# Kernel optimization log

Measured on AMD Instinct MI355X. Metric: run time of the kernel, lower is better.

The kernel has to match this reference:

```python
import jax, jax.numpy as jnp
import numpy as np

HID, D, NH, NL = 1024, 64, 16, 128  # hidden_dim, head_dim, num_head, num_landmarks


def iterative_inv(mat, n_iter=6):
    # Moore-Penrose pseudo-inverse via Newton-Schulz (Nystromformer), fp32.
    I = jnp.eye(mat.shape[-1], dtype=mat.dtype)
    K = mat
    denom = (jnp.max(jnp.sum(jnp.abs(K), axis=-2), axis=-1)
             * jnp.max(jnp.sum(jnp.abs(K), axis=-1), axis=-1))[..., None, None]
    V = jnp.swapaxes(K, -1, -2) / denom  # Z0 = K^T / (||K||_1 ||K||_inf)
    for _ in range(n_iter):
        KV = K @ V
        V = 0.25 * V @ (13.0 * I - KV @ (15.0 * I - KV @ (7.0 * I - KV)))
    return V


def nystrom_forward(X, mask, Wq, bq, Wk, bk, Wv, bv, Wo, bo):
    B, orig_len, _ = X.shape
    pad_len = NL - orig_len % NL  # always >= 1, matches torch code
    L = orig_len + pad_len
    Xp = jnp.pad(X, ((0, 0), (0, pad_len), (0, 0)))

    def split(Y):  # [B, L, NH*D] -> [B, NH, L, D]
        return Y.reshape(B, L, NH, D).transpose(0, 2, 1, 3)

    Q = split(Xp @ Wq.T + bq).astype(jnp.float32)
    K = split(Xp @ Wk.T + bk).astype(jnp.float32)
    V = split(Xp @ Wv.T + bv).astype(jnp.float32)

    m = mask[:, None, :, None]  # [B,1,L,1]
    scale = 1.0 / (D ** 0.25)   # 1/sqrt(sqrt(head_dim)) applied to both Q and K
    Q = Q * m * scale
    K = K * m * scale

    seg = L // NL
    Q_l = Q.reshape(B, NH, NL, seg, D).mean(axis=-2)  # landmarks via segment means
    K_l = K.reshape(B, NH, NL, seg, D).mean(axis=-2)

    kernel_1 = jax.nn.softmax(jnp.einsum('bhnd,bhld->bhnl', Q, K_l), axis=-1)   # [B,H,L,NL]
    kernel_2 = jax.nn.softmax(jnp.einsum('bhld,bhmd->bhlm', Q_l, K_l), axis=-1)  # [B,H,NL,NL]
    scores_3 = jnp.einsum('bhld,bhnd->bhln', Q_l, K) - 1e9 * (1.0 - mask[:, None, None, :])
    kernel_3 = jax.nn.softmax(scores_3, axis=-1)                                 # [B,H,NL,L]

    out = kernel_1 @ (iterative_inv(kernel_2) @ (kernel_3 @ V))  # [B,H,L,D]
    out = out.transpose(0, 2, 1, 3).reshape(B, L, NH * D)
    out = out @ Wo.T + bo
    return out[:, :orig_len]


def setup_inputs() -> dict:
    key = jax.random.key(0)
    ks = jax.random.split(key, 9)
    B, S = 2, 4095
    Lpad = S + (NL - S % NL)
    s = 0.02
    return {
        'X': jax.random.normal(ks[0], (B, S, HID), dtype=jnp.float32),
        'mask': jnp.ones((B, Lpad), dtype=jnp.float32),
        'Wq': jax.random.normal(ks[1], (NH * D, HID), dtype=jnp.float32) * s,
        'bq': jnp.zeros((NH * D,), dtype=jnp.float32),
        'Wk': jax.random.normal(ks[2], (NH * D, HID), dtype=jnp.float32) * s,
        'bk': jnp.zeros((NH * D,), dtype=jnp.float32),
        'Wv': jax.random.normal(ks[3], (NH * D, HID), dtype=jnp.float32) * s,
        'bv': jnp.zeros((NH * D,), dtype=jnp.float32),
        'Wo': jax.random.normal(ks[4], (HID, NH * D), dtype=jnp.float32) * s,
        'bo': jnp.zeros((HID,), dtype=jnp.float32),
    }


def reference(X, mask, Wq, bq, Wk, bk, Wv, bv, Wo, bo):
    return nystrom_forward(X, mask, Wq, bq, Wk, bk, Wv, bv, Wo, bo)
```

## Files before the change

kernel.cpp:

```cpp
#include <hip/hip_runtime.h>
#include <hip/hip_bf16.h>
#include <math.h>

#define S_ORIG 4095
#define LPAD   4096
#define NHEADS 16
#define DH     64
#define NLM    128
#define BHT    32
#define HIDDEN 1024
#define QKSCALE 0.35355339059327373f

typedef unsigned short u16;
typedef short s16x8 __attribute__((ext_vector_type(8)));
typedef float f32x4 __attribute__((ext_vector_type(4)));

#define IDX64(r, c)  ((r) * 64 + ((c) ^ (((r) & 7) << 3)))
#define IDX128(r, c) ((r) * 128 + ((c) ^ (((r) & 7) << 3)))

__device__ inline void split2(float x, u16& h, u16& l) {
    __hip_bfloat16 bh = __float2bfloat16(x);
    float fh = __bfloat162float(bh);
    __hip_bfloat16 bl = __float2bfloat16(x - fh);
    h = *(u16*)&bh;
    l = *(u16*)&bl;
}

__global__ __launch_bounds__(256) void k_split_x(const float* __restrict__ X,
                                                 u16* __restrict__ XH,
                                                 u16* __restrict__ XL) {
    int idx = blockIdx.x * 256 + threadIdx.x;
    int gr = idx >> 8;
    int c4 = (idx & 255) * 4;
    int b = gr >> 12, l = gr & (LPAD - 1);
    float4 v = make_float4(0.f, 0.f, 0.f, 0.f);
    if (l < S_ORIG) v = *(const float4*)(X + ((size_t)b * S_ORIG + l) * HIDDEN + c4);
    ushort4 h4, l4;
    split2(v.x, h4.x, l4.x); split2(v.y, h4.y, l4.y);
    split2(v.z, h4.z, l4.z); split2(v.w, h4.w, l4.w);
    size_t o = (size_t)gr * HIDDEN + c4;
    *(ushort4*)(XH + o) = h4;
    *(ushort4*)(XL + o) = l4;
}

__global__ __launch_bounds__(256) void k_split_w(const float* __restrict__ W,
                                                 u16* __restrict__ WH,
                                                 u16* __restrict__ WL) {
    int idx = blockIdx.x * 256 + threadIdx.x;
    size_t o = (size_t)idx * 4;
    float4 v = *(const float4*)(W + o);
    ushort4 h4, l4;
    split2(v.x, h4.x, l4.x); split2(v.y, h4.y, l4.y);
    split2(v.z, h4.z, l4.z); split2(v.w, h4.w, l4.w);
    *(ushort4*)(WH + o) = h4;
    *(ushort4*)(WL + o) = l4;
}

__global__ __launch_bounds__(256) void k_gemm_bf16(
    const u16* __restrict__ AH, const u16* __restrict__ AL,
    const u16* __restrict__ BH, const u16* __restrict__ BL,
    const float* __restrict__ bias, const float* __restrict__ mask,
    float* __restrict__ out, int mode)
{
    __shared__ u16 Ah_lds[128 * 32];
    __shared__ u16 Al_lds[128 * 32];
    __shared__ u16 Bh_lds[128 * 32];
    __shared__ u16 Bl_lds[128 * 32];
    int tid = threadIdx.x;
    int row0 = blockIdx.x * 128, col0 = blockIdx.y * 128;
    int lane = tid & 63, wv = tid >> 6;
    int wr = (wv >> 1) * 64, wc = (wv & 1) * 64;
    int lr = lane & 15, lk = lane >> 4;
    int sr = tid >> 2, sc = tid & 3;

    f32x4 acc[4][4] = {};

    for (int kt = 0; kt < 1024; kt += 32) {
        #pragma unroll
        for (int h = 0; h < 2; ++h) {
            int r = sr + h * 64;
            int csrc = (sc ^ ((r >> 1) & 3)) * 8;
            size_t ga = (size_t)(row0 + r) * HIDDEN + kt + csrc;
            size_t gb = (size_t)(col0 + r) * HIDDEN + kt + csrc;
            int ldst = r * 32 + sc * 8;
            __builtin_amdgcn_global_load_lds(
                (const __attribute__((address_space(1))) void*)(AH + ga),
                (__attribute__((address_space(3))) void*)(&Ah_lds[ldst]), 16, 0, 0);
            __builtin_amdgcn_global_load_lds(
                (const __attribute__((address_space(1))) void*)(AL + ga),
                (__attribute__((address_space(3))) void*)(&Al_lds[ldst]), 16, 0, 0);
            __builtin_amdgcn_global_load_lds(
                (const __attribute__((address_space(1))) void*)(BH + gb),
                (__attribute__((address_space(3))) void*)(&Bh_lds[ldst]), 16, 0, 0);
            __builtin_amdgcn_global_load_lds(
                (const __attribute__((address_space(1))) void*)(BL + gb),
                (__attribute__((address_space(3))) void*)(&Bl_lds[ldst]), 16, 0, 0);
        }
        __syncthreads();
        s16x8 ah[4], al[4], bh[4], bl[4];
        #pragma unroll
        for (int i = 0; i < 4; ++i) {
            int ra = wr + i * 16 + lr;
            int rb = wc + i * 16 + lr;
            int ca = (lk ^ ((ra >> 1) & 3)) * 8;
            int cb = (lk ^ ((rb >> 1) & 3)) * 8;
            ah[i] = *(const s16x8*)&Ah_lds[ra * 32 + ca];
            al[i] = *(const s16x8*)&Al_lds[ra * 32 + ca];
            bh[i] = *(const s16x8*)&Bh_lds[rb * 32 + cb];
            bl[i] = *(const s16x8*)&Bl_lds[rb * 32 + cb];
        }
        #pragma unroll
        for (int i = 0; i < 4; ++i)
            #pragma unroll
            for (int j = 0; j < 4; ++j)
                acc[i][j] = __builtin_amdgcn_mfma_f32_16x16x32_bf16(ah[i], bh[j], acc[i][j], 0, 0, 0);
        #pragma unroll
        for (int i = 0; i < 4; ++i)
            #pragma unroll
            for (int j = 0; j < 4; ++j)
                acc[i][j] = __builtin_amdgcn_mfma_f32_16x16x32_bf16(ah[i], bl[j], acc[i][j], 0, 0, 0);
        #pragma unroll
        for (int i = 0; i < 4; ++i)
            #pragma unroll
            for (int j = 0; j < 4; ++j)
                acc[i][j] = __builtin_amdgcn_mfma_f32_16x16x32_bf16(al[i], bh[j], acc[i][j], 0, 0, 0);
        __syncthreads();
    }

    #pragma unroll
    for (int i = 0; i < 4; ++i) {
        #pragma unroll
        for (int j = 0; j < 4; ++j) {
            int cc = col0 + wc + j * 16 + lr;
            float bval = bias[cc];
            #pragma unroll
            for (int q = 0; q < 4; ++q) {
                int rr = row0 + wr + i * 16 + lk * 4 + q;
                int bb = rr >> 12, l = rr & (LPAD - 1);
                float val = acc[i][j][q] + bval;
                if (mode == 0) {
                    if (mask) val *= mask[(size_t)bb * LPAD + l] * QKSCALE;
                    out[(((size_t)bb * NHEADS + (cc >> 6)) * LPAD + l) * DH + (cc & 63)] = val;
                } else {
                    if (l < S_ORIG)
                        out[((size_t)bb * S_ORIG + l) * HIDDEN + cc] = val;
                }
            }
        }
    }
}

__global__ void k_landmarks(const float* __restrict__ Q, const float* __restrict__ K,
                            float* __restrict__ QL, float* __restrict__ KL) {
    int n = blockIdx.x, bh = blockIdx.y, d = threadIdx.x;
    size_t base = ((size_t)bh * LPAD + n * 32) * DH + d;
    float sq = 0.f, sk = 0.f;
    #pragma unroll
    for (int s = 0; s < 32; ++s) {
        sq += Q[base + (size_t)s * DH];
        sk += K[base + (size_t)s * DH];
    }
    QL[((size_t)bh * NLM + n) * DH + d] = sq * (1.f / 32.f);
    KL[((size_t)bh * NLM + n) * DH + d] = sk * (1.f / 32.f);
}

__global__ __launch_bounds__(256) void k_qlk(const float* __restrict__ QLb,
                                             const float* __restrict__ Bsrc,
                                             float* __restrict__ out) {
    __shared__ float Qt[64][132];
    __shared__ float Bt[64][132];
    int tid = threadIdx.x;
    int tx = tid & 15, ty = tid >> 4;
    int bh = blockIdx.y;
    const float* QLp = QLb + (size_t)bh * NLM * DH;
    const float* Bp = Bsrc + (size_t)bh * NLM * DH;

    #pragma unroll
    for (int q = 0; q < 8; ++q) {
        int idx = tid + q * 256;
        int r = idx >> 4, d4 = idx & 15;
        float4 v = *(const float4*)(QLp + (size_t)r * DH + d4 * 4);
        Qt[d4 * 4 + 0][r] = v.x; Qt[d4 * 4 + 1][r] = v.y;
        Qt[d4 * 4 + 2][r] = v.z; Qt[d4 * 4 + 3][r] = v.w;
        float4 w = *(const float4*)(Bp + (size_t)r * DH + d4 * 4);
        Bt[d4 * 4 + 0][r] = w.x; Bt[d4 * 4 + 1][r] = w.y;
        Bt[d4 * 4 + 2][r] = w.z; Bt[d4 * 4 + 3][r] = w.w;
    }
    __syncthreads();

    float acc[8][8];
    #pragma unroll
    for (int i = 0; i < 8; ++i)
        #pragma unroll
        for (int j = 0; j < 8; ++j) acc[i][j] = 0.f;

    #pragma unroll
    for (int k = 0; k < 64; ++k) {
        float av[8], bv[8];
        float4 t0 = *(const float4*)&Qt[k][ty * 4];
        float4 t1 = *(const float4*)&Qt[k][64 + ty * 4];
        float4 t2 = *(const float4*)&Bt[k][tx * 4];
        float4 t3 = *(const float4*)&Bt[k][64 + tx * 4];
        av[0]=t0.x; av[1]=t0.y; av[2]=t0.z; av[3]=t0.w;
        av[4]=t1.x; av[5]=t1.y; av[6]=t1.z; av[7]=t1.w;
        bv[0]=t2.x; bv[1]=t2.y; bv[2]=t2.z; bv[3]=t2.w;
        bv[4]=t3.x; bv[5]=t3.y; bv[6]=t3.z; bv[7]=t3.w;
        #pragma unroll
        for (int i = 0; i < 8; ++i)
            #pragma unroll
            for (int j = 0; j < 8; ++j)
                acc[i][j] = fmaf(av[i], bv[j], acc[i][j]);
    }

    float m[8], s[8];
    #pragma unroll
    for (int i = 0; i < 8; ++i) {
        m[i] = acc[i][0];
        #pragma unroll
        for (int j = 1; j < 8; ++j) m[i] = fmaxf(m[i], acc[i][j]);
    }
    #pragma unroll
    for (int o = 8; o >= 1; o >>= 1)
        #pragma unroll
        for (int i = 0; i < 8; ++i) m[i] = fmaxf(m[i], __shfl_xor(m[i], o));
    #pragma unroll
    for (int i = 0; i < 8; ++i) {
        s[i] = 0.f;
        #pragma unroll
        for (int j = 0; j < 8; ++j) {
            acc[i][j] = expf(acc[i][j] - m[i]);
            s[i] += acc[i][j];
        }
    }
    #pragma unroll
    for (int o = 8; o >= 1; o >>= 1)
        #pragma unroll
        for (int i = 0; i < 8; ++i) s[i] += __shfl_xor(s[i], o);
    #pragma unroll
    for (int i = 0; i < 8; ++i) {
        int r = (i >> 2) * 64 + ty * 4 + (i & 3);
        float inv = 1.f / s[i];
        #pragma unroll
        for (int jh = 0; jh < 2; ++jh) {
            int c = jh * 64 + tx * 4;
            float4 res;
            res.x = acc[i][jh * 4 + 0] * inv;
            res.y = acc[i][jh * 4 + 1] * inv;
            res.z = acc[i][jh * 4 + 2] * inv;
            res.w = acc[i][jh * 4 + 3] * inv;
            *(float4*)(out + ((size_t)bh * NLM + r) * NLM + c) = res;
        }
    }
}

__global__ void k_v0denom(const float* __restrict__ K2b, float* __restrict__ V0b) {
    int bh = blockIdx.x, t = threadIdx.x;
    const float* K2 = K2b + (size_t)bh * NLM * NLM;
    float* V0 = V0b + (size_t)bh * NLM * NLM;
    float cs = 0.f, rs = 0.f;
    for (int r = 0; r < NLM; ++r) cs += fabsf(K2[r * NLM + t]);
    for (int c = 0; c < NLM; ++c) rs += fabsf(K2[t * NLM + c]);
    __shared__ float sc[128], sr[128];
    sc[t] = cs; sr[t] = rs;
    __syncthreads();
    for (int s = 64; s > 0; s >>= 1) {
        if (t < s) {
            sc[t] = fmaxf(sc[t], sc[t + s]);
            sr[t] = fmaxf(sr[t], sr[t + s]);
        }
        __syncthreads();
    }
    float invden = 1.f / (sc[0] * sr[0]);
    for (int idx = t; idx < NLM * NLM; idx += 128) {
        int i = idx >> 7, j = idx & 127;
        V0[idx] = K2[j * NLM + i] * invden;
    }
}

__global__ __launch_bounds__(256) void k_bmm(const float* __restrict__ Ab,
                                             const float* __restrict__ Bb,
                                             float* __restrict__ Cb,
                                             float* __restrict__ C2b,
                                             int N, float alpha, float sI,
                                             float alpha2, float sI2) {
    __shared__ float At[128][68];
    __shared__ float Bs[128][68];
    int tid = threadIdx.x;
    int tx = tid & 15, ty = tid >> 4;
    int bh = blockIdx.z;
    int r0 = blockIdx.y * 64, c0 = blockIdx.x * 64;
    const float* A = Ab + (size_t)bh * NLM * NLM;
    const float* Bm = Bb + (size_t)bh * NLM * N;

    #pragma unroll
    for (int q = 0; q < 8; ++q) {
        int idx = tid + q * 256;
        int r = idx >> 5, k4 = idx & 31;
        float4 v = *(const float4*)(A + (size_t)(r0 + r) * NLM + k4 * 4);
        At[k4 * 4 + 0][r] = v.x; At[k4 * 4 + 1][r] = v.y;
        At[k4 * 4 + 2][r] = v.z; At[k4 * 4 + 3][r] = v.w;
        int bk = idx >> 4, c4 = idx & 15;
        float4 w = *(const float4*)(Bm + (size_t)bk * N + c0 + c4 * 4);
        *(float4*)&Bs[bk][c4 * 4] = w;
    }
    __syncthreads();

    float acc[4][4];
    #pragma unroll
    for (int i = 0; i < 4; ++i)
        #pragma unroll
        for (int j = 0; j < 4; ++j) acc[i][j] = 0.f;

    #pragma unroll 4
    for (int k = 0; k < 128; ++k) {
        float4 a = *(const float4*)&At[k][ty * 4];
        float4 b = *(const float4*)&Bs[k][tx * 4];
        float av[4] = {a.x, a.y, a.z, a.w};
        float bv[4] = {b.x, b.y, b.z, b.w};
        #pragma unroll
        for (int i = 0; i < 4; ++i)
            #pragma unroll
            for (int j = 0; j < 4; ++j)
                acc[i][j] = fmaf(av[i], bv[j], acc[i][j]);
    }

    float* C = Cb + (size_t)bh * NLM * N;
    float* C2 = C2b ? (C2b + (size_t)bh * NLM * N) : nullptr;
    #pragma unroll
    for (int i = 0; i < 4; ++i) {
        int gr = r0 + ty * 4 + i;
        int gc0 = c0 + tx * 4;
        float4 res, res2;
        float* rp = &res.x; float* rp2 = &res2.x;
        #pragma unroll
        for (int j = 0; j < 4; ++j) {
            float idadd = (gr == gc0 + j) ? 1.f : 0.f;
            rp[j] = alpha * acc[i][j] + sI * idadd;
            rp2[j] = alpha2 * acc[i][j] + sI2 * idadd;
        }
        *(float4*)(C + (size_t)gr * N + gc0) = res;
        if (C2) *(float4*)(C2 + (size_t)gr * N + gc0) = res2;
    }
}

__global__ __launch_bounds__(256) void k_flashk3(const float* __restrict__ QLb,
                                                 const float* __restrict__ K,
                                                 const float* __restrict__ V,
                                                 const float* __restrict__ mask,
                                                 float* __restrict__ PO,
                                                 float* __restrict__ ML) {
    __shared__ u16 lds[57344];
    u16* QLh = lds;
    u16* QLl = lds + 4096;
    u16* Kh  = lds + 8192;
    u16* Kl  = lds + 16384;
    u16* Vth = lds + 24576;
    u16* Vtl = lds + 32768;
    u16* Ph  = lds + 40960;
    u16* Pl  = lds + 49152;

    int tid = threadIdx.x;
    int lane = tid & 63, wv = tid >> 6;
    int lr = lane & 15, lk = lane >> 4;
    int sp = blockIdx.x, qh = blockIdx.y, bh = blockIdx.z;
    int b = bh >> 4;
    int q0 = qh * 64;
    int wr16 = wv * 16;

    #pragma unroll
    for (int q = 0; q < 2; ++q) {
        int idx = tid + q * 256;
        int r = idx >> 3, c8 = (idx & 7) * 8;
        const float* src = QLb + ((size_t)bh * NLM + q0 + r) * DH + c8;
        float4 v0 = *(const float4*)src;
        float4 v1 = *(const float4*)(src + 4);
        float xs[8] = {v0.x, v0.y, v0.z, v0.w, v1.x, v1.y, v1.z, v1.w};
        s16x8 h8, l8;
        #pragma unroll
        for (int e = 0; e < 8; ++e) {
            u16 hh2, ll2; split2(xs[e], hh2, ll2);
            h8[e] = (short)hh2; l8[e] = (short)ll2;
        }
        *(s16x8*)&QLh[IDX64(r, c8)] = h8;
        *(s16x8*)&QLl[IDX64(r, c8)] = l8;
    }

    float m_run[4] = {-1e30f, -1e30f, -1e30f, -1e30f};
    float l_run[4] = {0.f, 0.f, 0.f, 0.f};
    f32x4 t5[4] = {};

    for (int t = 0; t < 4; ++t) {
        int kt0 = sp * 512 + t * 128;
        #pragma unroll
        for (int q = 0; q < 4; ++q) {
            int idx = tid + q * 256;
            int r = idx >> 3, c8 = (idx & 7) * 8;
            const float* src = K + ((size_t)bh * LPAD + kt0 + r) * DH + c8;
            float4 v0 = *(const float4*)src;
            float4 v1 = *(const float4*)(src + 4);
            float xs[8] = {v0.x, v0.y, v0.z, v0.w, v1.x, v1.y, v1.z, v1.w};
            s16x8 h8, l8;
            #pragma unroll
            for (int e = 0; e < 8; ++e) {
                u16 hh2, ll2; split2(xs[e], hh2, ll2);
                h8[e] = (short)hh2; l8[e] = (short)ll2;
            }
            *(s16x8*)&Kh[IDX64(r, c8)] = h8;
            *(s16x8*)&Kl[IDX64(r, c8)] = l8;
        }
        #pragma unroll
        for (int q = 0; q < 8; ++q) {
            int idx = tid + q * 256;
            int n = idx >> 4, d4 = (idx & 15) * 4;
            float4 v = *(const float4*)(V + ((size_t)bh * LPAD + kt0 + n) * DH + d4);
            float xs[4] = {v.x, v.y, v.z, v.w};
            #pragma unroll
            for (int e = 0; e < 4; ++e) {
                u16 hh2, ll2; split2(xs[e], hh2, ll2);
                Vth[IDX128(d4 + e, n)] = hh2;
                Vtl[IDX128(d4 + e, n)] = ll2;
            }
        }
        __syncthreads();

        f32x4 t4[8] = {};
        #pragma unroll
        for (int tt = 0; tt < 3; ++tt) {
            const u16* Xs = (tt == 2) ? QLl : QLh;
            const u16* Ys = (tt == 1) ? Kl : Kh;
            #pragma unroll
            for (int kc = 0; kc < 2; ++kc) {
                s16x8 a = *(const s16x8*)&Xs[IDX64(wr16 + lr, kc * 32 + lk * 8)];
                s16x8 bfr[8];
                #pragma unroll
                for (int j = 0; j < 8; ++j)
                    bfr[j] = *(const s16x8*)&Ys[IDX64(j * 16 + lr, kc * 32 + lk * 8)];
                #pragma unroll
                for (int j = 0; j < 8; ++j)
                    t4[j] = __builtin_amdgcn_mfma_f32_16x16x32_bf16(a, bfr[j], t4[j], 0, 0, 0);
            }
        }

        #pragma unroll
        for (int j = 0; j < 8; ++j) {
            float pen = 1e9f * (1.f - mask[(size_t)b * LPAD + kt0 + j * 16 + lr]);
            #pragma unroll
            for (int q = 0; q < 4; ++q) t4[j][q] -= pen;
        }

        float alpha[4];
        #pragma unroll
        for (int q = 0; q < 4; ++q) {
            float tm = t4[0][q];
            #pragma unroll
            for (int j = 1; j < 8; ++j) tm = fmaxf(tm, t4[j][q]);
            tm = fmaxf(tm, __shfl_xor(tm, 1));
            tm = fmaxf(tm, __shfl_xor(tm, 2));
            tm = fmaxf(tm, __shfl_xor(tm, 4));
            tm = fmaxf(tm, __shfl_xor(tm, 8));
            float mn = fmaxf(m_run[q], tm);
            float al = expf(m_run[q] - mn);
            float s = 0.f;
            #pragma unroll
            for (int j = 0; j < 8; ++j) {
                t4[j][q] = expf(t4[j][q] - mn);
                s += t4[j][q];
            }
            s += __shfl_xor(s, 1);
            s += __shfl_xor(s, 2);
            s += __shfl_xor(s, 4);
            s += __shfl_xor(s, 8);
            l_run[q] = l_run[q] * al + s;
            m_run[q] = mn;
            alpha[q] = al;
        }
        #pragma unroll
        for (int j = 0; j < 4; ++j)
            #pragma unroll
            for (int q = 0; q < 4; ++q) t5[j][q] *= alpha[q];

        #pragma unroll
        for (int j = 0; j < 8; ++j) {
            int col = j * 16 + lr;
            #pragma unroll
            for (int q = 0; q < 4; ++q) {
                int row = wr16 + lk * 4 + q;
                u16 hh2, ll2; split2(t4[j][q], hh2, ll2);
                Ph[IDX128(row, col)] = hh2;
                Pl[IDX128(row, col)] = ll2;
            }
        }
        __syncthreads();

        #pragma unroll
        for (int tt = 0; tt < 3; ++tt) {
            const u16* Xs = (tt == 2) ? Pl : Ph;
            const u16* Ys = (tt == 1) ? Vtl : Vth;
            #pragma unroll
            for (int kc = 0; kc < 4; ++kc) {
                s16x8 a = *(const s16x8*)&Xs[IDX128(wr16 + lr, kc * 32 + lk * 8)];
                s16x8 bfr[4];
                #pragma unroll
                for (int j = 0; j < 4; ++j)
                    bfr[j] = *(const s16x8*)&Ys[IDX128(j * 16 + lr, kc * 32 + lk * 8)];
                #pragma unroll
                for (int j = 0; j < 4; ++j)
                    t5[j] = __builtin_amdgcn_mfma_f32_16x16x32_bf16(a, bfr[j], t5[j], 0, 0, 0);
            }
        }
        __syncthreads();
    }

    size_t pb = (size_t)(bh * 16 + qh * 8 + sp) * 64;
    #pragma unroll
    for (int j = 0; j < 4; ++j) {
        int d = j * 16 + lr;
        #pragma unroll
        for (int q = 0; q < 4; ++q) {
            int row = wr16 + lk * 4 + q;
            PO[(pb + row) * 64 + d] = t5[j][q];
        }
    }
    if (lr == 0) {
        #pragma unroll
        for (int q = 0; q < 4; ++q) {
            int row = wr16 + lk * 4 + q;
            ML[(pb + row) * 2 + 0] = m_run[q];
            ML[(pb + row) * 2 + 1] = l_run[q];
        }
    }
}

__global__ void k_flash_combine(const float* __restrict__ PO,
                                const float* __restrict__ ML,
                                float* __restrict__ K3V) {
    int idx = blockIdx.x * 256 + threadIdx.x;
    int bh = idx >> 13, rem = idx & 8191;
    int g = rem >> 6, d = rem & 63;
    int qh = g >> 6, rl = g & 63;
    size_t rb = (size_t)(bh * 16 + qh * 8) * 64 + rl;
    float mstar = -1e30f;
    #pragma unroll
    for (int sp = 0; sp < 8; ++sp)
        mstar = fmaxf(mstar, ML[(rb + (size_t)sp * 64) * 2]);
    float osum = 0.f, lsum = 0.f;
    #pragma unroll
    for (int sp = 0; sp < 8; ++sp) {
        size_t r = rb + (size_t)sp * 64;
        float wgt = expf(ML[r * 2] - mstar);
        osum += wgt * PO[r * 64 + d];
        lsum += wgt * ML[r * 2 + 1];
    }
    K3V[idx] = osum / lsum;
}

__global__ __launch_bounds__(256) void k_attn(const float* __restrict__ Q,
                                              const float* __restrict__ KLb,
                                              const float* __restrict__ MMb,
                                              u16* __restrict__ ATH,
                                              u16* __restrict__ ATL) {
    __shared__ u16 lds[49152];
    u16* Qh  = lds;
    u16* Ql  = lds + 8192;
    u16* KLh = lds + 16384;
    u16* KLl = lds + 24576;
    u16* Ph  = lds;
    u16* Pl  = lds + 16384;
    u16* Mth = lds + 32768;
    u16* Mtl = lds + 40960;

    int tid = threadIdx.x;
    int lane = tid & 63, wv = tid >> 6;
    int lr = lane & 15, lk = lane >> 4;
    int l0 = blockIdx.x * 128, bh = blockIdx.y;
    int b = bh >> 4, hh = bh & 15;
    int wrA = wv * 32;

    #pragma unroll
    for (int q = 0; q < 4; ++q) {
        int idx = tid + q * 256;
        int r = idx >> 3, c8 = (idx & 7) * 8;
        float4 v0 = *(const float4*)(Q + ((size_t)bh * LPAD + l0 + r) * DH + c8);
        float4 v1 = *(const float4*)(Q + ((size_t)bh * LPAD + l0 + r) * DH + c8 + 4);
        float xs[8] = {v0.x, v0.y, v0.z, v0.w, v1.x, v1.y, v1.z, v1.w};
        s16x8 h8, l8;
        #pragma unroll
        for (int e = 0; e < 8; ++e) {
            u16 hh2, ll2; split2(xs[e], hh2, ll2);
            h8[e] = (short)hh2; l8[e] = (short)ll2;
        }
        *(s16x8*)&Qh[IDX64(r, c8)] = h8;
        *(s16x8*)&Ql[IDX64(r, c8)] = l8;

        float4 w0 = *(const float4*)(KLb + ((size_t)bh * NLM + r) * DH + c8);
        float4 w1 = *(const float4*)(KLb + ((size_t)bh * NLM + r) * DH + c8 + 4);
        float ys[8] = {w0.x, w0.y, w0.z, w0.w, w1.x, w1.y, w1.z, w1.w};
        #pragma unroll
        for (int e = 0; e < 8; ++e) {
            u16 hh2, ll2; split2(ys[e], hh2, ll2);
            h8[e] = (short)hh2; l8[e] = (short)ll2;
        }
        *(s16x8*)&KLh[IDX64(r, c8)] = h8;
        *(s16x8*)&KLl[IDX64(r, c8)] = l8;
    }
    #pragma unroll
    for (int q = 0; q < 8; ++q) {
        int idx = tid + q * 256;
        int n = idx >> 4, d4 = (idx & 15) * 4;
        float4 v = *(const float4*)(MMb + ((size_t)bh * NLM + n) * DH + d4);
        float xs[4] = {v.x, v.y, v.z, v.w};
        #pragma unroll
        for (int e = 0; e < 4; ++e) {
            u16 hh2, ll2; split2(xs[e], hh2, ll2);
            Mth[IDX128(d4 + e, n)] = hh2;
            Mtl[IDX128(d4 + e, n)] = ll2;
        }
    }
    __syncthreads();

    f32x4 t4[2][8] = {};
    #pragma unroll
    for (int t = 0; t < 3; ++t) {
        const u16* Xs = (t == 2) ? Ql : Qh;
        const u16* Ys = (t == 1) ? KLl : KLh;
        #pragma unroll
        for (int kc = 0; kc < 2; ++kc) {
            s16x8 a[2], bfr[8];
            #pragma unroll
            for (int i = 0; i < 2; ++i)
                a[i] = *(const s16x8*)&Xs[IDX64(wrA + i * 16 + lr, kc * 32 + lk * 8)];
            #pragma unroll
            for (int j = 0; j < 8; ++j)
                bfr[j] = *(const s16x8*)&Ys[IDX64(j * 16 + lr, kc * 32 + lk * 8)];
            #pragma unroll
            for (int i = 0; i < 2; ++i)
                #pragma unroll
                for (int j = 0; j < 8; ++j)
                    t4[i][j] = __builtin_amdgcn_mfma_f32_16x16x32_bf16(a[i], bfr[j], t4[i][j], 0, 0, 0);
        }
    }

    #pragma unroll
    for (int i = 0; i < 2; ++i)
        #pragma unroll
        for (int q = 0; q < 4; ++q) {
            float m = t4[i][0][q];
            #pragma unroll
            for (int j = 1; j < 8; ++j) m = fmaxf(m, t4[i][j][q]);
            m = fmaxf(m, __shfl_xor(m, 1));
            m = fmaxf(m, __shfl_xor(m, 2));
            m = fmaxf(m, __shfl_xor(m, 4));
            m = fmaxf(m, __shfl_xor(m, 8));
            float s = 0.f;
            #pragma unroll
            for (int j = 0; j < 8; ++j) {
                t4[i][j][q] = expf(t4[i][j][q] - m);
                s += t4[i][j][q];
            }
            s += __shfl_xor(s, 1);
            s += __shfl_xor(s, 2);
            s += __shfl_xor(s, 4);
            s += __shfl_xor(s, 8);
            float inv = 1.f / s;
            #pragma unroll
            for (int j = 0; j < 8; ++j) t4[i][j][q] *= inv;
        }

    __syncthreads();
    #pragma unroll
    for (int i = 0; i < 2; ++i)
        #pragma unroll
        for (int j = 0; j < 8; ++j) {
            int col = j * 16 + lr;
            #pragma unroll
            for (int q = 0; q < 4; ++q) {
                int row = wrA + i * 16 + lk * 4 + q;
                u16 hh2, ll2; split2(t4[i][j][q], hh2, ll2);
                Ph[IDX128(row, col)] = hh2;
                Pl[IDX128(row, col)] = ll2;
            }
        }
    __syncthreads();

    f32x4 t5[2][4] = {};
    #pragma unroll
    for (int t = 0; t < 3; ++t) {
        const u16* Xs = (t == 2) ? Pl : Ph;
        const u16* Ys = (t == 1) ? Mtl : Mth;
        #pragma unroll
        for (int kc = 0; kc < 4; ++kc) {
            s16x8 a[2], bfr[4];
            #pragma unroll
            for (int i = 0; i < 2; ++i)
                a[i] = *(const s16x8*)&Xs[IDX128(wrA + i * 16 + lr, kc * 32 + lk * 8)];
            #pragma unroll
            for (int j = 0; j < 4; ++j)
                bfr[j] = *(const s16x8*)&Ys[IDX128(j * 16 + lr, kc * 32 + lk * 8)];
            #pragma unroll
            for (int i = 0; i < 2; ++i)
                #pragma unroll
                for (int j = 0; j < 4; ++j)
                    t5[i][j] = __builtin_amdgcn_mfma_f32_16x16x32_bf16(a[i], bfr[j], t5[i][j], 0, 0, 0);
        }
    }

    #pragma unroll
    for (int i = 0; i < 2; ++i)
        #pragma unroll
        for (int j = 0; j < 4; ++j) {
            int d = j * 16 + lr;
            #pragma unroll
            for (int q = 0; q < 4; ++q) {
                int l = l0 + wrA + i * 16 + lk * 4 + q;
                size_t base = ((size_t)b * LPAD + l) * HIDDEN + hh * DH + d;
                u16 hh2, ll2; split2(t5[i][j][q], hh2, ll2);
                ATH[base] = hh2;
                ATL[base] = ll2;
            }
        }
}

extern "C" void kernel_launch(void* const* d_in, const int* in_sizes, int n_in,
                              void* d_out, int out_size, void* d_ws, size_t ws_size,
                              hipStream_t stream) {
    (void)in_sizes; (void)n_in; (void)out_size; (void)ws_size;
    const float* X    = (const float*)d_in[0];
    const float* mask = (const float*)d_in[1];
    const float* Wq   = (const float*)d_in[2];
    const float* bq   = (const float*)d_in[3];
    const float* Wk   = (const float*)d_in[4];
    const float* bk   = (const float*)d_in[5];
    const float* Wv   = (const float*)d_in[6];
    const float* bv   = (const float*)d_in[7];
    const float* Wo   = (const float*)d_in[8];
    const float* bo   = (const float*)d_in[9];
    float* out = (float*)d_out;
    float* w = (float*)d_ws;

    size_t o = 0;
    u16* WQH = (u16*)(w + o); o += (size_t)HIDDEN * HIDDEN / 2;
    u16* WQL = (u16*)(w + o); o += (size_t)HIDDEN * HIDDEN / 2;
    u16* WKH = (u16*)(w + o); o += (size_t)HIDDEN * HIDDEN / 2;
    u16* WKL = (u16*)(w + o); o += (size_t)HIDDEN * HIDDEN / 2;
    u16* WVH = (u16*)(w + o); o += (size_t)HIDDEN * HIDDEN / 2;
    u16* WVL = (u16*)(w + o); o += (size_t)HIDDEN * HIDDEN / 2;
    u16* WOH = (u16*)(w + o); o += (size_t)HIDDEN * HIDDEN / 2;
    u16* WOL = (u16*)(w + o); o += (size_t)HIDDEN * HIDDEN / 2;
    float* Q   = w + o; o += (size_t)BHT * LPAD * DH;
    float* K   = w + o; o += (size_t)BHT * LPAD * DH;
    float* V   = w + o; o += (size_t)BHT * LPAD * DH;
    float* QL  = w + o; o += (size_t)BHT * NLM * DH;
    float* KL  = w + o; o += (size_t)BHT * NLM * DH;
    float* K2  = w + o; o += (size_t)BHT * NLM * NLM;
    float* VA  = w + o; o += (size_t)BHT * NLM * NLM;
    float* VB  = w + o; o += (size_t)BHT * NLM * NLM;
    float* KV  = w + o; o += (size_t)BHT * NLM * NLM;
    float* P1  = w + o; o += (size_t)BHT * NLM * NLM;
    float* T3  = w + o; o += (size_t)BHT * NLM * NLM;
    float* PK  = w + o; o += (size_t)BHT * 16 * NLM * DH;
    float* K3V = w + o; o += (size_t)BHT * NLM * DH;
    float* MM  = w + o; o += (size_t)BHT * NLM * DH;
    float* SC  = w + o; o += (size_t)BHT * NLM * LPAD;

    float* PO = PK;
    float* ML = PK + (size_t)BHT * 16 * 64 * 64;

    u16* XH  = (u16*)SC;
    u16* XL  = XH + (size_t)2 * LPAD * HIDDEN;
    u16* ATH = (u16*)SC;
    u16* ATL = ATH + (size_t)2 * LPAD * HIDDEN;

    k_split_x<<<8192, 256, 0, stream>>>(X, XH, XL);
    k_split_w<<<1024, 256, 0, stream>>>(Wq, WQH, WQL);
    k_split_w<<<1024, 256, 0, stream>>>(Wk, WKH, WKL);
    k_split_w<<<1024, 256, 0, stream>>>(Wv, WVH, WVL);
    k_split_w<<<1024, 256, 0, stream>>>(Wo, WOH, WOL);

    dim3 gg(64, 8);
    k_gemm_bf16<<<gg, 256, 0, stream>>>(XH, XL, WQH, WQL, bq, mask, Q, 0);
    k_gemm_bf16<<<gg, 256, 0, stream>>>(XH, XL, WKH, WKL, bk, mask, K, 0);
    k_gemm_bf16<<<gg, 256, 0, stream>>>(XH, XL, WVH, WVL, bv, nullptr, V, 0);

    k_landmarks<<<dim3(NLM, BHT), 64, 0, stream>>>(Q, K, QL, KL);

    k_qlk<<<dim3(1, BHT), 256, 0, stream>>>(QL, KL, K2);

    k_flashk3<<<dim3(8, 2, BHT), 256, 0, stream>>>(QL, K, V, mask, PO, ML);
    k_flash_combine<<<(BHT * NLM * DH) / 256, 256, 0, stream>>>(PO, ML, K3V);

    k_v0denom<<<BHT, 128, 0, stream>>>(K2, VA);
    float* cur = VA;
    float* nxt = VB;
    for (int it = 0; it < 6; ++it) {
        k_bmm<<<dim3(2, 2, BHT), 256, 0, stream>>>(K2, cur, KV, P1, NLM, 1.f, 0.f, -1.f, 7.f);
        k_bmm<<<dim3(2, 2, BHT), 256, 0, stream>>>(KV, P1, T3, nullptr, NLM, -1.f, 15.f, 0.f, 0.f);
        k_bmm<<<dim3(2, 2, BHT), 256, 0, stream>>>(KV, T3, P1, nullptr, NLM, -1.f, 13.f, 0.f, 0.f);
        k_bmm<<<dim3(2, 2, BHT), 256, 0, stream>>>(cur, P1, nxt, nullptr, NLM, 0.25f, 0.f, 0.f, 0.f);
        float* t = cur; cur = nxt; nxt = t;
    }

    k_bmm<<<dim3(1, 2, BHT), 256, 0, stream>>>(cur, K3V, MM, nullptr, DH, 1.f, 0.f, 0.f, 0.f);

    k_attn<<<dim3(32, BHT), 256, 0, stream>>>(Q, KL, MM, ATH, ATL);
    k_gemm_bf16<<<gg, 256, 0, stream>>>(ATH, ATL, WOH, WOL, bo, nullptr, out, 1);
}
```

Measured before the change: 645.2 us.

## Emit K/V as pre-split bf16 hi/lo pairs and DMA them into LDS in flash kernel

The K and V projection GEMMs now write their outputs directly as bf16 high/low halves instead of fp32. The landmark kernel reconstructs K from those halves and also writes pre-split Q landmarks. The flash kernel_3 pass then loads the QL and K tiles with global_load_lds DMA, using the swizzle applied on the source side, and loads V as ushort4. This removes the repeated fp32-to-bf16 splitting and halves the global read traffic in the flash loop. The cost is extra split work in the GEMM epilogue, scattered 2-byte stores there, and a K landmark computed from the reconstructed hi+lo value rather than the exact fp32.

```diff
diff --git a/kernel.cpp b/kernel.cpp
--- a/kernel.cpp
+++ b/kernel.cpp
@@ -24,6 +24,11 @@
     __hip_bfloat16 bl = __float2bfloat16(x - fh);
     h = *(u16*)&bh;
     l = *(u16*)&bl;
+}
+
+__device__ inline float bf16f(u16 b) {
+    unsigned u = ((unsigned)b) << 16;
+    return *(float*)&u;
 }
 
 __global__ __launch_bounds__(256) void k_split_x(const float* __restrict__ X,
@@ -60,7 +65,8 @@
     const u16* __restrict__ AH, const u16* __restrict__ AL,
     const u16* __restrict__ BH, const u16* __restrict__ BL,
     const float* __restrict__ bias, const float* __restrict__ mask,
-    float* __restrict__ out, int mode)
+    float* __restrict__ out, u16* __restrict__ poutH, u16* __restrict__ poutL,
+    int mode)
 {
     __shared__ u16 Ah_lds[128 * 32];
     __shared__ u16 Al_lds[128 * 32];
@@ -140,7 +146,14 @@
                 float val = acc[i][j][q] + bval;
                 if (mode == 0) {
                     if (mask) val *= mask[(size_t)bb * LPAD + l] * QKSCALE;
-                    out[(((size_t)bb * NHEADS + (cc >> 6)) * LPAD + l) * DH + (cc & 63)] = val;
+                    size_t oi = (((size_t)bb * NHEADS + (cc >> 6)) * LPAD + l) * DH + (cc & 63);
+                    if (poutH) {
+                        u16 hh2, ll2; split2(val, hh2, ll2);
+                        poutH[oi] = hh2;
+                        poutL[oi] = ll2;
+                    } else {
+                        out[oi] = val;
+                    }
                 } else {
                     if (l < S_ORIG)
                         out[((size_t)bb * S_ORIG + l) * HIDDEN + cc] = val;
@@ -150,18 +163,25 @@
     }
 }
 
-__global__ void k_landmarks(const float* __restrict__ Q, const float* __restrict__ K,
-                            float* __restrict__ QL, float* __restrict__ KL) {
+__global__ void k_landmarks(const float* __restrict__ Q,
+                            const u16* __restrict__ KPH, const u16* __restrict__ KPL,
+                            float* __restrict__ QL, float* __restrict__ KL,
+                            u16* __restrict__ QLPH, u16* __restrict__ QLPL) {
     int n = blockIdx.x, bh = blockIdx.y, d = threadIdx.x;
     size_t base = ((size_t)bh * LPAD + n * 32) * DH + d;
     float sq = 0.f, sk = 0.f;
     #pragma unroll
     for (int s = 0; s < 32; ++s) {
         sq += Q[base + (size_t)s * DH];
-        sk += K[base + (size_t)s * DH];
-    }
-    QL[((size_t)bh * NLM + n) * DH + d] = sq * (1.f / 32.f);
-    KL[((size_t)bh * NLM + n) * DH + d] = sk * (1.f / 32.f);
+        sk += bf16f(KPH[base + (size_t)s * DH]) + bf16f(KPL[base + (size_t)s * DH]);
+    }
+    float ql = sq * (1.f / 32.f), kl = sk * (1.f / 32.f);
+    size_t oi = ((size_t)bh * NLM + n) * DH + d;
+    QL[oi] = ql;
+    KL[oi] = kl;
+    u16 hh2, ll2; split2(ql, hh2, ll2);
+    QLPH[oi] = hh2;
+    QLPL[oi] = ll2;
 }
 
 __global__ __launch_bounds__(256) void k_qlk(const float* __restrict__ QLb,
@@ -343,9 +363,12 @@
     }
 }
 
-__global__ __launch_bounds__(256) void k_flashk3(const float* __restrict__ QLb,
-                                                 const float* __restrict__ K,
-                                                 const float* __restrict__ V,
+__global__ __launch_bounds__(256) void k_flashk3(const u16* __restrict__ QLPH,
+                                                 const u16* __restrict__ QLPL,
+                                                 const u16* __restrict__ KPH,
+                                                 const u16* __restrict__ KPL,
+                                                 const u16* __restrict__ VPH,
+                                                 const u16* __restrict__ VPL,
                                                  const float* __restrict__ mask,
                                                  float* __restrict__ PO,
                                                  float* __restrict__ ML) {
@@ -370,19 +393,15 @@
     #pragma unroll
     for (int q = 0; q < 2; ++q) {
         int idx = tid + q * 256;
-        int r = idx >> 3, c8 = (idx & 7) * 8;
-        const float* src = QLb + ((size_t)bh * NLM + q0 + r) * DH + c8;
-        float4 v0 = *(const float4*)src;
-        float4 v1 = *(const float4*)(src + 4);
-        float xs[8] = {v0.x, v0.y, v0.z, v0.w, v1.x, v1.y, v1.z, v1.w};
-        s16x8 h8, l8;
-        #pragma unroll
-        for (int e = 0; e < 8; ++e) {
-            u16 hh2, ll2; split2(xs[e], hh2, ll2);
-            h8[e] = (short)hh2; l8[e] = (short)ll2;
-        }
-        *(s16x8*)&QLh[IDX64(r, c8)] = h8;
-        *(s16x8*)&QLl[IDX64(r, c8)] = l8;
+        int r = idx >> 3, sc = idx & 7;
+        int csrc = (sc ^ (r & 7)) * 8;
+        size_t g = ((size_t)bh * NLM + q0 + r) * DH + csrc;
+        __builtin_amdgcn_global_load_lds(
+            (const __attribute__((address_space(1))) void*)(QLPH + g),
+            (__attribute__((address_space(3))) void*)(&QLh[idx * 8]), 16, 0, 0);
+        __builtin_amdgcn_global_load_lds(
+            (const __attribute__((address_space(1))) void*)(QLPL + g),
+            (__attribute__((address_space(3))) void*)(&QLl[idx * 8]), 16, 0, 0);
     }
 
     float m_run[4] = {-1e30f, -1e30f, -1e30f, -1e30f};
@@ -394,31 +413,28 @@
         #pragma unroll
         for (int q = 0; q < 4; ++q) {
             int idx = tid + q * 256;
-            int r = idx >> 3, c8 = (idx & 7) * 8;
-            const float* src = K + ((size_t)bh * LPAD + kt0 + r) * DH + c8;
-            float4 v0 = *(const float4*)src;
-            float4 v1 = *(const float4*)(src + 4);
-            float xs[8] = {v0.x, v0.y, v0.z, v0.w, v1.x, v1.y, v1.z, v1.w};
-            s16x8 h8, l8;
-            #pragma unroll
-            for (int e = 0; e < 8; ++e) {
-                u16 hh2, ll2; split2(xs[e], hh2, ll2);
-                h8[e] = (short)hh2; l8[e] = (short)ll2;
-            }
-            *(s16x8*)&Kh[IDX64(r, c8)] = h8;
-            *(s16x8*)&Kl[IDX64(r, c8)] = l8;
+            int r = idx >> 3, sc = idx & 7;
+            int csrc = (sc ^ (r & 7)) * 8;
+            size_t g = ((size_t)bh * LPAD + kt0 + r) * DH + csrc;
+            __builtin_amdgcn_global_load_lds(
+                (const __attribute__((address_space(1))) void*)(KPH + g),
+                (__attribute__((address_space(3))) void*)(&Kh[idx * 8]), 16, 0, 0);
+            __builtin_amdgcn_global_load_lds(
+                (const __attribute__((address_space(1))) void*)(KPL + g),
+                (__attribute__((address_space(3))) void*)(&Kl[idx * 8]), 16, 0, 0);
         }
         #pragma unroll
         for (int q = 0; q < 8; ++q) {
             int idx = tid + q * 256;
-            int n = idx >> 4, d4 = (idx & 15) * 4;
-            float4 v = *(const float4*)(V + ((size_t)bh * LPAD + kt0 + n) * DH + d4);
-            float xs[4] = {v.x, v.y, v.z, v.w};
+            int n = idx & 127, dg = idx >> 7;
+            int d4 = dg * 4;
+            size_t g = ((size_t)bh * LPAD + kt0 + n) * DH + d4;
+            ushort4 h4 = *(const ushort4*)(VPH + g);
+            ushort4 l4 = *(const ushort4*)(VPL + g);
             #pragma unroll
             for (int e = 0; e < 4; ++e) {
-                u16 hh2, ll2; split2(xs[e], hh2, ll2);
-                Vth[IDX128(d4 + e, n)] = hh2;
-                Vtl[IDX128(d4 + e, n)] = ll2;
+                Vth[IDX128(d4 + e, n)] = (&h4.x)[e];
+                Vtl[IDX128(d4 + e, n)] = (&l4.x)[e];
             }
         }
         __syncthreads();
@@ -762,6 +778,11 @@
     float* MM  = w + o; o += (size_t)BHT * NLM * DH;
     float* SC  = w + o; o += (size_t)BHT * NLM * LPAD;
 
+    u16* KPH = (u16*)K;
+    u16* KPL = KPH + (size_t)BHT * LPAD * DH;
+    u16* VPH = (u16*)V;
+    u16* VPL = VPH + (size_t)BHT * LPAD * DH;
+
     float* PO = PK;
     float* ML = PK + (size_t)BHT * 16 * 64 * 64;
 
@@ -769,6 +790,8 @@
     u16* XL  = XH + (size_t)2 * LPAD * HIDDEN;
     u16* ATH = (u16*)SC;
     u16* ATL = ATH + (size_t)2 * LPAD * HIDDEN;
+    u16* QLPH = (u16*)SC + (size_t)32 * 1024 * 1024;
+    u16* QLPL = QLPH + (size_t)BHT * NLM * DH;
 
     k_split_x<<<8192, 256, 0, stream>>>(X, XH, XL);
     k_split_w<<<1024, 256, 0, stream>>>(Wq, WQH, WQL);
@@ -777,15 +800,15 @@
     k_split_w<<<1024, 256, 0, stream>>>(Wo, WOH, WOL);
 
     dim3 gg(64, 8);
-    k_gemm_bf16<<<gg, 256, 0, stream>>>(XH, XL, WQH, WQL, bq, mask, Q, 0);
-    k_gemm_bf16<<<gg, 256, 0, stream>>>(XH, XL, WKH, WKL, bk, mask, K, 0);
-    k_gemm_bf16<<<gg, 256, 0, stream>>>(XH, XL, WVH, WVL, bv, nullptr, V, 0);
-
-    k_landmarks<<<dim3(NLM, BHT), 64, 0, stream>>>(Q, K, QL, KL);
+    k_gemm_bf16<<<gg, 256, 0, stream>>>(XH, XL, WQH, WQL, bq, mask, Q, nullptr, nullptr, 0);
+    k_gemm_bf16<<<gg, 256, 0, stream>>>(XH, XL, WKH, WKL, bk, mask, nullptr, KPH, KPL, 0);
+    k_gemm_bf16<<<gg, 256, 0, stream>>>(XH, XL, WVH, WVL, bv, nullptr, nullptr, VPH, VPL, 0);
+
+    k_landmarks<<<dim3(NLM, BHT), 64, 0, stream>>>(Q, KPH, KPL, QL, KL, QLPH, QLPL);
 
     k_qlk<<<dim3(1, BHT), 256, 0, stream>>>(QL, KL, K2);
 
-    k_flashk3<<<dim3(8, 2, BHT), 256, 0, stream>>>(QL, K, V, mask, PO, ML);
+    k_flashk3<<<dim3(8, 2, BHT), 256, 0, stream>>>(QLPH, QLPL, KPH, KPL, VPH, VPL, mask, PO, ML);
     k_flash_combine<<<(BHT * NLM * DH) / 256, 256, 0, stream>>>(PO, ML, K3V);
 
     k_v0denom<<<BHT, 128, 0, stream>>>(K2, VA);
@@ -802,5 +825,5 @@
     k_bmm<<<dim3(1, 2, BHT), 256, 0, stream>>>(cur, K3V, MM, nullptr, DH, 1.f, 0.f, 0.f, 0.f);
 
     k_attn<<<dim3(32, BHT), 256, 0, stream>>>(Q, KL, MM, ATH, ATL);
-    k_gemm_bf16<<<gg, 256, 0, stream>>>(ATH, ATL, WOH, WOL, bo, nullptr, out, 1);
-}
+    k_gemm_bf16<<<gg, 256, 0, stream>>>(ATH, ATL, WOH, WOL, bo, nullptr, out, nullptr, nullptr, 1);
+}
```

Result: no change. 637.6 us (-1.2%).
